# Optimization experiments

Hardware: AMD Instinct MI355X
Metric: run time of the kernel (lower is better)

## Reference

```python
import jax, jax.numpy as jnp
import numpy as np

N = 4096        # nodes
F_IN = 256      # in_features
F_OUT = 64      # out_features
H = 64          # lstm_out_features
MAX_DEG = 64    # max neighbor count == max packed seq length
ALPHA = 0.2     # leaky relu negative slope
NEG = -9e15


def setup_inputs() -> dict:
    key = jax.random.key(0)
    ks = jax.random.split(key, 8)
    h = jax.random.normal(ks[0], (N, F_IN), dtype=jnp.float32)
    # per-node neighbor counts in [1, MAX_DEG]
    seq_length = jax.random.randint(ks[1], (N,), 1, MAX_DEG + 1, dtype=jnp.int32)
    # adjacency with exactly seq_length[i] ones in row i
    r = jax.random.uniform(ks[2], (N, N))
    ranks = jnp.argsort(jnp.argsort(-r, axis=1), axis=1)
    adj = (ranks < seq_length[:, None]).astype(jnp.float32)
    # parameters (xavier-ish scale)
    W = jax.random.normal(ks[3], (F_IN, F_OUT), dtype=jnp.float32) * (2.0 / (F_IN + F_OUT)) ** 0.5
    a = jax.random.normal(ks[4], (2 * F_OUT, 1), dtype=jnp.float32) * 0.1
    # backward-direction LSTM weights (torch gate order i,f,g,o); forward dir is unused in output
    w_ih = jax.random.normal(ks[5], (4 * H, F_OUT), dtype=jnp.float32) * 0.1
    w_hh = jax.random.normal(ks[6], (4 * H, H), dtype=jnp.float32) * 0.1
    b_ih = jnp.zeros((4 * H,), dtype=jnp.float32)
    b_hh = jnp.zeros((4 * H,), dtype=jnp.float32)
    return {"h": h, "adj": adj, "seq_length": seq_length, "W": W, "a": a,
            "w_ih": w_ih, "w_hh": w_hh, "b_ih": b_ih, "b_hh": b_hh}


def reference(h, adj, seq_length, W, a, w_ih, w_hh, b_ih, b_hh):
    n = h.shape[0]
    Wh = h @ W                                   # [N, F_OUT]
    # e[i,j] = leakyrelu(a_left . Wh_i + a_right . Wh_j)  (same math as O(N^2) concat)
    a1, a2 = a[:F_OUT, 0], a[F_OUT:, 0]
    e = jax.nn.leaky_relu((Wh @ a1)[:, None] + (Wh @ a2)[None, :], negative_slope=ALPHA)
    att = jax.nn.softmax(jnp.where(adj > 0, e, NEG), axis=1)   # [N, N]
    Wh2 = att @ Wh                               # aggregated node features [N, F_OUT]
    # sort neighbors by descending attention; LSTM only reads the first seq_length[i] <= MAX_DEG
    order = jnp.argsort(-att, axis=1)[:, :MAX_DEG]            # [N, T]
    seq = Wh2[order]                              # [N, T, F_OUT]
    # backward LSTM direction == run forward over the length-reversed sequence
    t = jnp.arange(MAX_DEG)
    rev_idx = jnp.clip(seq_length[:, None] - 1 - t[None, :], 0)
    rev = jnp.take_along_axis(seq, rev_idx[:, :, None], axis=1)  # [N, T, F_OUT]
    mask = t[None, :] < seq_length[:, None]                       # [N, T]

    def cell(carry, xm):
        hs, cs = carry
        x, m = xm                                 # x: [N, F_OUT], m: [N]
        gates = x @ w_ih.T + hs @ w_hh.T + b_ih + b_hh
        i, f, g, o = jnp.split(gates, 4, axis=1)
        c_new = jax.nn.sigmoid(f) * cs + jax.nn.sigmoid(i) * jnp.tanh(g)
        h_new = jax.nn.sigmoid(o) * jnp.tanh(c_new)
        m = m[:, None]
        return (jnp.where(m, h_new, hs), jnp.where(m, c_new, cs)), None

    init = (jnp.zeros((n, H), Wh.dtype), jnp.zeros((n, H), Wh.dtype))
    xs = (jnp.swapaxes(rev, 0, 1), mask.T)        # time-major
    (hn, _), _ = jax.lax.scan(cell, init, xs)
    return hn                                     # [N, H]  == torch hn[-1] (backward dir)
```

## Files before the change

### kernel.cpp

```cpp
#include <hip/hip_runtime.h>
#include <hip/hip_bf16.h>
#include <math.h>

#define N_NODES 4096
#define F_INN   256
#define F_OUTT  64
#define HID     64
#define MAXDEG  64

typedef __attribute__((ext_vector_type(8))) short bf16x8;
typedef __attribute__((ext_vector_type(4))) float f32x4;

__device__ int    g_mode;
__device__ int    g_anyArr[64];
__device__ float  g_Wh [N_NODES * F_OUTT];
__device__ float  g_s1 [N_NODES];
__device__ float  g_s2 [N_NODES];
__device__ int    g_rev[N_NODES * MAXDEG];
__device__ int    g_perm[N_NODES];
__device__ int    g_nbr[N_NODES * MAXDEG];
__device__ int    g_cnt[N_NODES];
__device__ float4 g_GX [N_NODES * F_OUTT];

__device__ __forceinline__ float bf2f(unsigned short u) {
  union { unsigned int i; float f; } v; v.i = ((unsigned int)u) << 16; return v.f;
}
__device__ __forceinline__ unsigned short f2bf(float f) {
  union { __hip_bfloat16 b; unsigned short u; } v; v.b = __float2bfloat16(f); return v.u;
}

__device__ __forceinline__ float bcastf(float v, int l) {
  return __int_as_float(__builtin_amdgcn_readlane(__float_as_int(v), l));
}

__device__ __forceinline__ float rcp_fast(float x) { return __builtin_amdgcn_rcpf(x); }

__device__ __forceinline__ float sigm(float x) {
  return rcp_fast(1.f + __expf(-x));
}
__device__ __forceinline__ float tanh_fast(float x) {
  return fmaf(-2.f, rcp_fast(1.f + __expf(2.f * x)), 1.f);
}

__device__ __forceinline__ int mbcnt64(unsigned long long m) {
  return __builtin_amdgcn_mbcnt_hi((unsigned)(m >> 32),
         __builtin_amdgcn_mbcnt_lo((unsigned)(m & 0xFFFFFFFFull), 0));
}

__device__ __forceinline__ bf16x8 zfrag() {
  bf16x8 z;
  #pragma unroll
  for (int i = 0; i < 8; i++) z[i] = 0;
  return z;
}

__device__ __forceinline__ void block_sync_lds() {
  __asm__ volatile("s_waitcnt lgkmcnt(0)" ::: "memory");
  __builtin_amdgcn_s_barrier();
}

#define MFMA16(a, b, c) __builtin_amdgcn_mfma_f32_16x16x32_bf16((a), (b), (c), 0, 0, 0)

__global__ __launch_bounds__(256) void k_detect(const unsigned int* __restrict__ aw) {
  __shared__ int any;
  if (threadIdx.x == 0) any = 0;
  __syncthreads();
  const uint4 v = ((const uint4*)aw)[blockIdx.x * 256 + threadIdx.x];
  int loc = (int)((v.x & 0xFFFFu) | (v.y & 0xFFFFu) | (v.z & 0xFFFFu) | (v.w & 0xFFFFu));
  if (loc) atomicOr(&any, 1);
  __syncthreads();
  if (threadIdx.x == 0) g_anyArr[blockIdx.x] = any;
}

__global__ __launch_bounds__(256) void k_sort(const int* __restrict__ seq) {
  __shared__ int hist[MAXDEG + 1];
  __shared__ int offs[MAXDEG + 1];
  const int tid = threadIdx.x;
  if (tid <= MAXDEG) hist[tid] = 0;
  __syncthreads();
  if (tid == 0) {
    int any = 0;
    for (int b = 0; b < 64; b++) any |= g_anyArr[b];
    g_mode = any ? 1 : 0;
  }
  for (int i = tid; i < N_NODES; i += 256)
    atomicAdd(&hist[min(max(seq[i], 0), MAXDEG)], 1);
  __syncthreads();
  if (tid == 0) {
    int run = 0;
    for (int L = MAXDEG; L >= 0; L--) { offs[L] = run; run += hist[L]; }
  }
  __syncthreads();
  for (int i = tid; i < N_NODES; i += 256) {
    int p = atomicAdd(&offs[min(max(seq[i], 0), MAXDEG)], 1);
    g_perm[p] = i;
  }
}

__global__ __launch_bounds__(256) void k_scan(const void* __restrict__ adj) {
  const bool bf16 = (g_mode == 1);
  const int i = blockIdx.x;
  const int w = threadIdx.x >> 6, lane = threadIdx.x & 63;
  __shared__ int seg[4][MAXDEG];
  __shared__ int scnt[4];

  int base = 0;
  if (bf16) {
    const uint4* ar = (const uint4*)((const unsigned short*)adj + (size_t)i * N_NODES);
    #pragma unroll
    for (int it = 0; it < 2; it++) {
      const uint4 v = ar[w * 128 + it * 64 + lane];
      unsigned word[4] = {v.x, v.y, v.z, v.w};
      bool nz[8];
      #pragma unroll
      for (int k = 0; k < 4; k++) {
        nz[2 * k]     = (word[k] & 0x0000FFFFu) != 0u;
        nz[2 * k + 1] = (word[k] & 0xFFFF0000u) != 0u;
      }
      int pre = 0, tot = 0;
      #pragma unroll
      for (int k = 0; k < 8; k++) {
        unsigned long long bl = __ballot(nz[k]);
        pre += mbcnt64(bl);
        tot += __popcll(bl);
      }
      int loc = 0;
      #pragma unroll
      for (int k = 0; k < 8; k++) {
        if (nz[k]) {
          int p = base + pre + loc;
          if (p < MAXDEG) seg[w][p] = w * 1024 + it * 512 + lane * 8 + k;
          loc++;
        }
      }
      base += tot;
    }
  } else {
    const float4* ar = (const float4*)((const float*)adj + (size_t)i * N_NODES);
    #pragma unroll
    for (int it = 0; it < 4; it++) {
      const float4 v = ar[w * 256 + it * 64 + lane];
      bool nz[4] = {v.x != 0.0f, v.y != 0.0f, v.z != 0.0f, v.w != 0.0f};
      int pre = 0, tot = 0;
      #pragma unroll
      for (int k = 0; k < 4; k++) {
        unsigned long long bl = __ballot(nz[k]);
        pre += mbcnt64(bl);
        tot += __popcll(bl);
      }
      int loc = 0;
      #pragma unroll
      for (int k = 0; k < 4; k++) {
        if (nz[k]) {
          int p = base + pre + loc;
          if (p < MAXDEG) seg[w][p] = w * 1024 + it * 256 + lane * 4 + k;
          loc++;
        }
      }
      base += tot;
    }
  }
  if (lane == 0) scnt[w] = base;
  __syncthreads();
  int off = 0;
  #pragma unroll
  for (int u = 0; u < 4; u++) off += (u < w) ? scnt[u] : 0;
  const int cw = min(scnt[w], MAXDEG);
  if (lane < cw) {
    const int p = off + lane;
    if (p < MAXDEG) g_nbr[i * MAXDEG + p] = seg[w][lane];
  }
  if (threadIdx.x == 0)
    g_cnt[i] = min(scnt[0] + scnt[1] + scnt[2] + scnt[3], MAXDEG);
}

__global__ __launch_bounds__(256) void k_wh(
    const void* __restrict__ h, const void* __restrict__ W, const void* __restrict__ a)
{
  const bool bf16 = (g_mode == 1);
  __shared__ float Ws[F_INN * F_OUTT];
  const int tid = threadIdx.x;
  if (bf16) {
    const ushort4* Wu = (const ushort4*)W;
    for (int v = tid; v < F_INN * F_OUTT / 4; v += 256) {
      ushort4 u = Wu[v];
      ((float4*)Ws)[v] = make_float4(bf2f(u.x), bf2f(u.y), bf2f(u.z), bf2f(u.w));
    }
  } else {
    const float4* Wf = (const float4*)W;
    for (int v = tid; v < F_INN * F_OUTT / 4; v += 256) ((float4*)Ws)[v] = Wf[v];
  }
  __syncthreads();
  const int wave = tid >> 6, lane = tid & 63;
  const int row = blockIdx.x * 4 + wave;
  float hr0, hr1, hr2, hr3;
  if (bf16) {
    ushort4 v = ((const ushort4*)((const unsigned short*)h + row * F_INN))[lane];
    hr0 = bf2f(v.x); hr1 = bf2f(v.y); hr2 = bf2f(v.z); hr3 = bf2f(v.w);
  } else {
    float4 v = ((const float4*)((const float*)h + row * F_INN))[lane];
    hr0 = v.x; hr1 = v.y; hr2 = v.z; hr3 = v.w;
  }
  double acc = 0.0;
  #pragma unroll 8
  for (int l = 0; l < 64; l++) {
    float h0 = bcastf(hr0, l), h1 = bcastf(hr1, l);
    float h2 = bcastf(hr2, l), h3 = bcastf(hr3, l);
    acc += (double)h0 * (double)Ws[(l * 4 + 0) * F_OUTT + lane];
    acc += (double)h1 * (double)Ws[(l * 4 + 1) * F_OUTT + lane];
    acc += (double)h2 * (double)Ws[(l * 4 + 2) * F_OUTT + lane];
    acc += (double)h3 * (double)Ws[(l * 4 + 3) * F_OUTT + lane];
  }
  const float whv = (float)acc;
  g_Wh[row * F_OUTT + lane] = whv;
  float a1, a2;
  if (bf16) {
    a1 = bf2f(((const unsigned short*)a)[lane]);
    a2 = bf2f(((const unsigned short*)a)[F_OUTT + lane]);
  } else {
    a1 = ((const float*)a)[lane];
    a2 = ((const float*)a)[F_OUTT + lane];
  }
  double t1 = (double)whv * (double)a1;
  double t2 = (double)whv * (double)a2;
  #pragma unroll
  for (int off = 32; off > 0; off >>= 1) {
    t1 += __shfl_down(t1, off);
    t2 += __shfl_down(t2, off);
  }
  if (lane == 0) { g_s1[row] = (float)t1; g_s2[row] = (float)t2; }
}

__global__ __launch_bounds__(256) void k_att2(
    const void* __restrict__ w_ih,
    const void* __restrict__ b_ih, const void* __restrict__ b_hh)
{
  const bool bf16 = (g_mode == 1);
  const int wv = threadIdx.x >> 6, lane = threadIdx.x & 63;
  const int i = blockIdx.x * 4 + wv;

  __shared__ int   s_nbr[4][MAXDEG];
  __shared__ float s_att[4][MAXDEG];
  __shared__ int   s_srt[4][MAXDEG];
  __shared__ float s_wh2[4][F_OUTT];
  int*   nbr  = s_nbr[wv];
  float* attp = s_att[wv];
  int*   srt  = s_srt[wv];
  float* wh2  = s_wh2[wv];

  const int L = min(g_cnt[i], MAXDEG);
  int jn = 0;
  if (lane < L) jn = g_nbr[i * MAXDEG + lane] & (N_NODES - 1);
  nbr[lane] = jn;

  const float s2v = g_s2[jn];
  float av;
  {
    float s = g_s1[i] + s2v;
    float e = (s > 0.0f) ? s : 0.2f * s;
    if (lane >= L) e = -3.0e38f;
    float m = e;
    #pragma unroll
    for (int off = 32; off > 0; off >>= 1) m = fmaxf(m, __shfl_xor(m, off));
    float p = (lane < L) ? __expf(e - m) : 0.0f;
    float ssum = p;
    #pragma unroll
    for (int off = 32; off > 0; off >>= 1) ssum += __shfl_xor(ssum, off);
    av = p * rcp_fast(ssum);
    attp[lane] = av;
    int rank = 0;
    for (int qq = 0; qq < L; qq++) {
      float aq = __shfl(av, qq);
      int   jq = __shfl(jn, qq);
      rank += (aq > av || (aq == av && jq < jn)) ? 1 : 0;
    }
    if (lane < L) srt[rank] = jn;
  }
  g_rev[i * MAXDEG + lane] = (lane < L) ? srt[L - 1 - lane] : 0;

  float a0 = 0.f, a1 = 0.f, a2 = 0.f, a3 = 0.f;
  int q = 0;
  for (; q + 4 <= L; q += 4) {
    const int j0 = nbr[q], j1 = nbr[q + 1], j2 = nbr[q + 2], j3 = nbr[q + 3];
    const float t0 = attp[q], t1 = attp[q + 1], t2 = attp[q + 2], t3 = attp[q + 3];
    a0 = fmaf(t0, g_Wh[(size_t)j0 * F_OUTT + lane], a0);
    a1 = fmaf(t1, g_Wh[(size_t)j1 * F_OUTT + lane], a1);
    a2 = fmaf(t2, g_Wh[(size_t)j2 * F_OUTT + lane], a2);
    a3 = fmaf(t3, g_Wh[(size_t)j3 * F_OUTT + lane], a3);
  }
  for (; q < L; q++) {
    const int j0 = nbr[q];
    a0 = fmaf(attp[q], g_Wh[(size_t)j0 * F_OUTT + lane], a0);
  }
  wh2[lane] = (a0 + a1) + (a2 + a3);

  float gx[4] = {0.f, 0.f, 0.f, 0.f};
  if (bf16) {
    #pragma unroll
    for (int g = 0; g < 4; g++) {
      const unsigned short* wr = (const unsigned short*)w_ih + (size_t)(g * 64 + lane) * F_OUTT;
      #pragma unroll
      for (int ch = 0; ch < 8; ch++) {
        bf16x8 vv = *(const bf16x8*)(wr + ch * 8);
        #pragma unroll
        for (int e2 = 0; e2 < 8; e2++)
          gx[g] = fmaf(bf2f((unsigned short)vv[e2]), wh2[ch * 8 + e2], gx[g]);
      }
      gx[g] += bf2f(((const unsigned short*)b_ih)[g * 64 + lane]) +
               bf2f(((const unsigned short*)b_hh)[g * 64 + lane]);
    }
  } else {
    #pragma unroll
    for (int g = 0; g < 4; g++) {
      const float* wr = (const float*)w_ih + (size_t)(g * 64 + lane) * F_OUTT;
      #pragma unroll
      for (int ch = 0; ch < 16; ch++) {
        float4 vv = *(const float4*)(wr + ch * 4);
        gx[g] = fmaf(vv.x, wh2[ch * 4 + 0], gx[g]);
        gx[g] = fmaf(vv.y, wh2[ch * 4 + 1], gx[g]);
        gx[g] = fmaf(vv.z, wh2[ch * 4 + 2], gx[g]);
        gx[g] = fmaf(vv.w, wh2[ch * 4 + 3], gx[g]);
      }
      gx[g] += ((const float*)b_ih)[g * 64 + lane] + ((const float*)b_hh)[g * 64 + lane];
    }
  }
  g_GX[(size_t)i * F_OUTT + lane] = make_float4(gx[0], gx[1], gx[2], gx[3]);
}

__global__ __launch_bounds__(256, 2) void k_lstm_mfma(
    const void* __restrict__ w_hh, const int* __restrict__ seq,
    void* __restrict__ out)
{
  const bool bf16 = (g_mode == 1);
  __shared__ __align__(16) unsigned short lds_h[2][16 * 72];
  __shared__ int lds_idx[8][MAXDEG];
  const int tid = threadIdx.x;
  const int w = tid >> 6, lane = tid & 63;
  const int q = lane >> 4, c = lane & 15;
  const int rb = blockIdx.x * 8;

  for (int v = tid; v < 2 * 16 * 72; v += 256) ((unsigned short*)lds_h)[v] = 0;

  for (int v = tid; v < 8 * MAXDEG; v += 256) {
    const int e = v >> 6, t0 = v & (MAXDEG - 1);
    const int row = g_perm[rb + e] & (N_NODES - 1);
    lds_idx[e][t0] = g_rev[row * MAXDEG + t0] & (N_NODES - 1);
  }

  const int Lmax = min(max(seq[g_perm[rb] & (N_NODES - 1)], 0), MAXDEG);

  int rows_c[4];
  #pragma unroll
  for (int r = 0; r < 4; r++) rows_c[r] = min(q * 4 + r, 7);

  int row_own[2], Ls_own[2];
  #pragma unroll
  for (int k = 0; k < 2; k++) {
    row_own[k] = g_perm[rb + 2 * q + k] & (N_NODES - 1);
    Ls_own[k]  = min(max(seq[row_own[k]], 0), MAXDEG);
  }
  const int d_unit = 16 * w + c;
  const int sl = ((lane >> 5) << 4) | c;
  const bool qodd = (q & 1) != 0;

  bf16x8 Bhi[4][2];
  #pragma unroll
  for (int g = 0; g < 4; g++) {
    const int col = 64 * g + d_unit;
    #pragma unroll
    for (int ch = 0; ch < 2; ch++) {
      if (bf16) {
        Bhi[g][ch] = *(const bf16x8*)((const unsigned short*)w_hh + (size_t)col * 64 + ch * 32 + q * 8);
      } else {
        const float* wp = (const float*)w_hh + (size_t)col * 64 + ch * 32 + q * 8;
        float4 va = *(const float4*)wp, vb = *(const float4*)(wp + 4);
        bf16x8 f;
        f[0] = (short)f2bf(va.x); f[1] = (short)f2bf(va.y);
        f[2] = (short)f2bf(va.z); f[3] = (short)f2bf(va.w);
        f[4] = (short)f2bf(vb.x); f[5] = (short)f2bf(vb.y);
        f[6] = (short)f2bf(vb.z); f[7] = (short)f2bf(vb.w);
        Bhi[g][ch] = f;
      }
    }
  }

  __syncthreads();

  float4 gxb[4][4];
  #pragma unroll
  for (int s = 0; s < 4; s++) {
    #pragma unroll
    for (int r = 0; r < 4; r++)
      gxb[s][r] = g_GX[lds_idx[rows_c[r]][s] * F_OUTT + d_unit];
  }
  int idx_cur[4];
  #pragma unroll
  for (int r = 0; r < 4; r++) idx_cur[r] = lds_idx[rows_c[r]][4];

  bf16x8 h0 = zfrag(), h1 = zfrag();
  float cst[2] = {0.f, 0.f}, hst[2] = {0.f, 0.f};
  const int Lr = (Lmax + 3) & ~3;

  for (int t = 0; t < Lr; t += 4) {
    #pragma unroll
    for (int j = 0; j < 4; j++) {
      const int tt = t + j;
      f32x4 acc[4];
      #pragma unroll
      for (int g = 0; g < 4; g++) {
        f32x4 a;
        a[0] = (g==0)?gxb[j][0].x:(g==1)?gxb[j][0].y:(g==2)?gxb[j][0].z:gxb[j][0].w;
        a[1] = (g==0)?gxb[j][1].x:(g==1)?gxb[j][1].y:(g==2)?gxb[j][1].z:gxb[j][1].w;
        a[2] = (g==0)?gxb[j][2].x:(g==1)?gxb[j][2].y:(g==2)?gxb[j][2].z:gxb[j][2].w;
        a[3] = (g==0)?gxb[j][3].x:(g==1)?gxb[j][3].y:(g==2)?gxb[j][3].z:gxb[j][3].w;
        a = MFMA16(h0, Bhi[g][0], a);
        a = MFMA16(h1, Bhi[g][1], a);
        acc[g] = a;
      }
      #pragma unroll
      for (int r = 0; r < 4; r++)
        gxb[j][r] = g_GX[idx_cur[r] * F_OUTT + d_unit];
      {
        const int nt = min(tt + 5, MAXDEG - 1);
        #pragma unroll
        for (int r = 0; r < 4; r++) idx_cur[r] = lds_idx[rows_c[r]][nt];
      }
      float gv[4][2];
      #pragma unroll
      for (int g = 0; g < 4; g++) {
        float t0v = __shfl(acc[g][0], sl);
        float t1v = __shfl(acc[g][1], sl);
        float t2v = __shfl(acc[g][2], sl);
        float t3v = __shfl(acc[g][3], sl);
        gv[g][0] = qodd ? t2v : t0v;
        gv[g][1] = qodd ? t3v : t1v;
      }
      unsigned short* lh = lds_h[j & 1];
      #pragma unroll
      for (int k = 0; k < 2; k++) {
        float ig = sigm(gv[0][k]);
        float fg = sigm(gv[1][k]);
        float gg = tanh_fast(gv[2][k]);
        float og = sigm(gv[3][k]);
        float cn = fg * cst[k] + ig * gg;
        float hn = og * tanh_fast(cn);
        bool live = (tt < Ls_own[k]);
        cst[k] = live ? cn : cst[k];
        hst[k] = live ? hn : hst[k];
        lh[(2 * q + k) * 72 + d_unit] = f2bf(hst[k]);
      }
      block_sync_lds();
      {
        const unsigned short* lr_ = lds_h[j & 1] + c * 72;
        h0 = *(const bf16x8*)(lr_ + 8 * q);
        h1 = *(const bf16x8*)(lr_ + 32 + 8 * q);
      }
    }
  }
  #pragma unroll
  for (int k = 0; k < 2; k++) {
    if (bf16) ((__hip_bfloat16*)out)[row_own[k] * HID + d_unit] = __float2bfloat16(hst[k]);
    else      ((float*)out)[row_own[k] * HID + d_unit] = hst[k];
  }
}

extern "C" void kernel_launch(void* const* d_in, const int* in_sizes, int n_in,
                              void* d_out, int out_size, void* d_ws, size_t ws_size,
                              hipStream_t stream) {
  (void)in_sizes; (void)n_in; (void)out_size; (void)d_ws; (void)ws_size;
  const void* h    = d_in[0];
  const void* adj  = d_in[1];
  const int*  seq  = (const int*)d_in[2];
  const void* W    = d_in[3];
  const void* a    = d_in[4];
  const void* w_ih = d_in[5];
  const void* w_hh = d_in[6];
  const void* b_ih = d_in[7];
  const void* b_hh = d_in[8];

  k_detect   <<<64,           256, 0, stream>>>((const unsigned int*)adj);
  k_sort     <<<1,            256, 0, stream>>>(seq);
  k_scan     <<<N_NODES,      256, 0, stream>>>(adj);
  k_wh       <<<N_NODES / 4,  256, 0, stream>>>(h, W, a);
  k_att2     <<<N_NODES / 4,  256, 0, stream>>>(w_ih, b_ih, b_hh);
  k_lstm_mfma<<<N_NODES / 8,  256, 0, stream>>>(w_hh, seq, d_out);
}
```

Baseline: 231.5 us.

## Register-block Wh matmul, pre-convert w_ih/bias, widen gather unroll

k_wh now computes four rows per wave, so each loaded W element is reused across four accumulators, and the grid shrinks by a factor of four. w_ih and the combined biases are converted to fp32 once inside k_scan and stored in globals, so k_att2 no longer converts bf16 or adds two biases per node. The neighbor gather in k_att2 is unrolled by eight, and the rank loop uses readlane instead of shuffles. These cut redundant W staging and conversion work, at the cost of more registers for the double accumulators and fewer blocks in k_wh.

After: 234.6 us. About the same (+1.3%).

```diff
diff --git a/kernel.cpp b/kernel.cpp
--- a/kernel.cpp
+++ b/kernel.cpp
@@ -20,6 +20,8 @@
 __device__ int    g_perm[N_NODES];
 __device__ int    g_nbr[N_NODES * MAXDEG];
 __device__ int    g_cnt[N_NODES];
+__device__ float  g_Wih[256 * F_OUTT];
+__device__ float  g_bias[256];
 __device__ float4 g_GX [N_NODES * F_OUTT];
 
 __device__ __forceinline__ float bf2f(unsigned short u) {
@@ -97,12 +99,25 @@
   }
 }
 
-__global__ __launch_bounds__(256) void k_scan(const void* __restrict__ adj) {
+__global__ __launch_bounds__(256) void k_scan(
+    const void* __restrict__ adj, const void* __restrict__ w_ih,
+    const void* __restrict__ b_ih, const void* __restrict__ b_hh)
+{
   const bool bf16 = (g_mode == 1);
   const int i = blockIdx.x;
   const int w = threadIdx.x >> 6, lane = threadIdx.x & 63;
   __shared__ int seg[4][MAXDEG];
   __shared__ int scnt[4];
+
+  if (i < 64) {
+    const int t = i * 256 + threadIdx.x;
+    g_Wih[t] = bf16 ? bf2f(((const unsigned short*)w_ih)[t]) : ((const float*)w_ih)[t];
+  } else if (i == 64) {
+    const int t = threadIdx.x;
+    g_bias[t] = bf16 ? (bf2f(((const unsigned short*)b_ih)[t]) +
+                        bf2f(((const unsigned short*)b_hh)[t]))
+                     : (((const float*)b_ih)[t] + ((const float*)b_hh)[t]);
+  }
 
   int base = 0;
   if (bf16) {
@@ -192,27 +207,32 @@
   }
   __syncthreads();
   const int wave = tid >> 6, lane = tid & 63;
-  const int row = blockIdx.x * 4 + wave;
-  float hr0, hr1, hr2, hr3;
-  if (bf16) {
-    ushort4 v = ((const ushort4*)((const unsigned short*)h + row * F_INN))[lane];
-    hr0 = bf2f(v.x); hr1 = bf2f(v.y); hr2 = bf2f(v.z); hr3 = bf2f(v.w);
-  } else {
-    float4 v = ((const float4*)((const float*)h + row * F_INN))[lane];
-    hr0 = v.x; hr1 = v.y; hr2 = v.z; hr3 = v.w;
-  }
-  double acc = 0.0;
-  #pragma unroll 8
+  const int row0 = blockIdx.x * 16 + wave * 4;
+
+  float hr[4][4];
+  #pragma unroll
+  for (int r = 0; r < 4; r++) {
+    if (bf16) {
+      ushort4 v = ((const ushort4*)((const unsigned short*)h + (row0 + r) * F_INN))[lane];
+      hr[0][r] = bf2f(v.x); hr[1][r] = bf2f(v.y); hr[2][r] = bf2f(v.z); hr[3][r] = bf2f(v.w);
+    } else {
+      float4 v = ((const float4*)((const float*)h + (row0 + r) * F_INN))[lane];
+      hr[0][r] = v.x; hr[1][r] = v.y; hr[2][r] = v.z; hr[3][r] = v.w;
+    }
+  }
+
+  double acc[4] = {0.0, 0.0, 0.0, 0.0};
+  #pragma unroll 4
   for (int l = 0; l < 64; l++) {
-    float h0 = bcastf(hr0, l), h1 = bcastf(hr1, l);
-    float h2 = bcastf(hr2, l), h3 = bcastf(hr3, l);
-    acc += (double)h0 * (double)Ws[(l * 4 + 0) * F_OUTT + lane];
-    acc += (double)h1 * (double)Ws[(l * 4 + 1) * F_OUTT + lane];
-    acc += (double)h2 * (double)Ws[(l * 4 + 2) * F_OUTT + lane];
-    acc += (double)h3 * (double)Ws[(l * 4 + 3) * F_OUTT + lane];
-  }
-  const float whv = (float)acc;
-  g_Wh[row * F_OUTT + lane] = whv;
+    #pragma unroll
+    for (int j = 0; j < 4; j++) {
+      const double wd = (double)Ws[(l * 4 + j) * F_OUTT + lane];
+      #pragma unroll
+      for (int r = 0; r < 4; r++)
+        acc[r] += (double)bcastf(hr[j][r], l) * wd;
+    }
+  }
+
   float a1, a2;
   if (bf16) {
     a1 = bf2f(((const unsigned short*)a)[lane]);
@@ -221,21 +241,23 @@
     a1 = ((const float*)a)[lane];
     a2 = ((const float*)a)[F_OUTT + lane];
   }
-  double t1 = (double)whv * (double)a1;
-  double t2 = (double)whv * (double)a2;
-  #pragma unroll
-  for (int off = 32; off > 0; off >>= 1) {
-    t1 += __shfl_down(t1, off);
-    t2 += __shfl_down(t2, off);
-  }
-  if (lane == 0) { g_s1[row] = (float)t1; g_s2[row] = (float)t2; }
-}
-
-__global__ __launch_bounds__(256) void k_att2(
-    const void* __restrict__ w_ih,
-    const void* __restrict__ b_ih, const void* __restrict__ b_hh)
-{
-  const bool bf16 = (g_mode == 1);
+
+  #pragma unroll
+  for (int r = 0; r < 4; r++) {
+    const float whv = (float)acc[r];
+    g_Wh[(row0 + r) * F_OUTT + lane] = whv;
+    double t1 = (double)whv * (double)a1;
+    double t2 = (double)whv * (double)a2;
+    #pragma unroll
+    for (int off = 32; off > 0; off >>= 1) {
+      t1 += __shfl_down(t1, off);
+      t2 += __shfl_down(t2, off);
+    }
+    if (lane == 0) { g_s1[row0 + r] = (float)t1; g_s2[row0 + r] = (float)t2; }
+  }
+}
+
+__global__ __launch_bounds__(256) void k_att2(void) {
   const int wv = threadIdx.x >> 6, lane = threadIdx.x & 63;
   const int i = blockIdx.x * 4 + wv;
 
@@ -270,8 +292,8 @@
     attp[lane] = av;
     int rank = 0;
     for (int qq = 0; qq < L; qq++) {
-      float aq = __shfl(av, qq);
-      int   jq = __shfl(jn, qq);
+      const float aq = bcastf(av, qq);
+      const int   jq = __builtin_amdgcn_readlane(jn, qq);
       rank += (aq > av || (aq == av && jq < jn)) ? 1 : 0;
     }
     if (lane < L) srt[rank] = jn;
@@ -279,50 +301,35 @@
   g_rev[i * MAXDEG + lane] = (lane < L) ? srt[L - 1 - lane] : 0;
 
   float a0 = 0.f, a1 = 0.f, a2 = 0.f, a3 = 0.f;
+  float a4 = 0.f, a5 = 0.f, a6 = 0.f, a7 = 0.f;
   int q = 0;
-  for (; q + 4 <= L; q += 4) {
-    const int j0 = nbr[q], j1 = nbr[q + 1], j2 = nbr[q + 2], j3 = nbr[q + 3];
-    const float t0 = attp[q], t1 = attp[q + 1], t2 = attp[q + 2], t3 = attp[q + 3];
-    a0 = fmaf(t0, g_Wh[(size_t)j0 * F_OUTT + lane], a0);
-    a1 = fmaf(t1, g_Wh[(size_t)j1 * F_OUTT + lane], a1);
-    a2 = fmaf(t2, g_Wh[(size_t)j2 * F_OUTT + lane], a2);
-    a3 = fmaf(t3, g_Wh[(size_t)j3 * F_OUTT + lane], a3);
-  }
-  for (; q < L; q++) {
-    const int j0 = nbr[q];
-    a0 = fmaf(attp[q], g_Wh[(size_t)j0 * F_OUTT + lane], a0);
-  }
-  wh2[lane] = (a0 + a1) + (a2 + a3);
+  for (; q + 8 <= L; q += 8) {
+    a0 = fmaf(attp[q    ], g_Wh[(size_t)nbr[q    ] * F_OUTT + lane], a0);
+    a1 = fmaf(attp[q + 1], g_Wh[(size_t)nbr[q + 1] * F_OUTT + lane], a1);
+    a2 = fmaf(attp[q + 2], g_Wh[(size_t)nbr[q + 2] * F_OUTT + lane], a2);
+    a3 = fmaf(attp[q + 3], g_Wh[(size_t)nbr[q + 3] * F_OUTT + lane], a3);
+    a4 = fmaf(attp[q + 4], g_Wh[(size_t)nbr[q + 4] * F_OUTT + lane], a4);
+    a5 = fmaf(attp[q + 5], g_Wh[(size_t)nbr[q + 5] * F_OUTT + lane], a5);
+    a6 = fmaf(attp[q + 6], g_Wh[(size_t)nbr[q + 6] * F_OUTT + lane], a6);
+    a7 = fmaf(attp[q + 7], g_Wh[(size_t)nbr[q + 7] * F_OUTT + lane], a7);
+  }
+  for (; q < L; q++)
+    a0 = fmaf(attp[q], g_Wh[(size_t)nbr[q] * F_OUTT + lane], a0);
+  wh2[lane] = ((a0 + a1) + (a2 + a3)) + ((a4 + a5) + (a6 + a7));
 
   float gx[4] = {0.f, 0.f, 0.f, 0.f};
-  if (bf16) {
-    #pragma unroll
-    for (int g = 0; g < 4; g++) {
-      const unsigned short* wr = (const unsigned short*)w_ih + (size_t)(g * 64 + lane) * F_OUTT;
-      #pragma unroll
-      for (int ch = 0; ch < 8; ch++) {
-        bf16x8 vv = *(const bf16x8*)(wr + ch * 8);
-        #pragma unroll
-        for (int e2 = 0; e2 < 8; e2++)
-          gx[g] = fmaf(bf2f((unsigned short)vv[e2]), wh2[ch * 8 + e2], gx[g]);
-      }
-      gx[g] += bf2f(((const unsigned short*)b_ih)[g * 64 + lane]) +
-               bf2f(((const unsigned short*)b_hh)[g * 64 + lane]);
-    }
-  } else {
-    #pragma unroll
-    for (int g = 0; g < 4; g++) {
-      const float* wr = (const float*)w_ih + (size_t)(g * 64 + lane) * F_OUTT;
-      #pragma unroll
-      for (int ch = 0; ch < 16; ch++) {
-        float4 vv = *(const float4*)(wr + ch * 4);
-        gx[g] = fmaf(vv.x, wh2[ch * 4 + 0], gx[g]);
-        gx[g] = fmaf(vv.y, wh2[ch * 4 + 1], gx[g]);
-        gx[g] = fmaf(vv.z, wh2[ch * 4 + 2], gx[g]);
-        gx[g] = fmaf(vv.w, wh2[ch * 4 + 3], gx[g]);
-      }
-      gx[g] += ((const float*)b_ih)[g * 64 + lane] + ((const float*)b_hh)[g * 64 + lane];
-    }
+  #pragma unroll
+  for (int g = 0; g < 4; g++) {
+    const float* wr = g_Wih + (size_t)(g * 64 + lane) * F_OUTT;
+    #pragma unroll
+    for (int ch = 0; ch < 16; ch++) {
+      float4 vv = *(const float4*)(wr + ch * 4);
+      gx[g] = fmaf(vv.x, wh2[ch * 4 + 0], gx[g]);
+      gx[g] = fmaf(vv.y, wh2[ch * 4 + 1], gx[g]);
+      gx[g] = fmaf(vv.z, wh2[ch * 4 + 2], gx[g]);
+      gx[g] = fmaf(vv.w, wh2[ch * 4 + 3], gx[g]);
+    }
+    gx[g] += g_bias[g * 64 + lane];
   }
   g_GX[(size_t)i * F_OUTT + lane] = make_float4(gx[0], gx[1], gx[2], gx[3]);
 }
@@ -480,8 +487,8 @@
 
   k_detect   <<<64,           256, 0, stream>>>((const unsigned int*)adj);
   k_sort     <<<1,            256, 0, stream>>>(seq);
-  k_scan     <<<N_NODES,      256, 0, stream>>>(adj);
-  k_wh       <<<N_NODES / 4,  256, 0, stream>>>(h, W, a);
-  k_att2     <<<N_NODES / 4,  256, 0, stream>>>(w_ih, b_ih, b_hh);
+  k_scan     <<<N_NODES,      256, 0, stream>>>(adj, w_ih, b_ih, b_hh);
+  k_wh       <<<N_NODES / 16, 256, 0, stream>>>(h, W, a);
+  k_att2     <<<N_NODES / 4,  256, 0, stream>>>();
   k_lstm_mfma<<<N_NODES / 8,  256, 0, stream>>>(w_hh, seq, d_out);
 }
```
